# Performance work log

Hardware: AMD Instinct MI355X
Metric: run time of the kernel (lower is better)

The kernel has to match this reference:

```python
import jax, jax.numpy as jnp
import numpy as np

N = 80000
E = 1280000
IN_DIM = 512
OUT_DIM = 64
POS_DIM = 8
NEG_SLOPE = 0.01  # F.leaky_relu default


def setup_inputs() -> dict:
    key = jax.random.key(0)
    k1, k2, k3, k4, k5, k6 = jax.random.split(key, 6)
    h = jax.random.normal(k1, (N, IN_DIM), dtype=jnp.float32)
    pos = jax.random.normal(k2, (N, POS_DIM), dtype=jnp.float32)
    src = jax.random.randint(k3, (E,), 0, N, dtype=jnp.int32)
    dst = jax.random.randint(k4, (E,), 0, N, dtype=jnp.int32)
    W_fc = jax.random.normal(k5, (OUT_DIM, IN_DIM), dtype=jnp.float32) * (1.0 / np.sqrt(IN_DIM))
    W_attn = jax.random.normal(k6, (1, 2 * OUT_DIM + 2 * POS_DIM), dtype=jnp.float32) * 0.1
    return {"h": h, "pos": pos, "src": src, "dst": dst, "W_fc": W_fc, "W_attn": W_attn}


def reference(h, pos, src, dst, W_fc, W_attn):
    # node projection: z = fc(h)  [N, out]
    z = h @ W_fc.T
    # attn_fc applied to concat([z_src, z_dst, pos_src, pos_dst]) == split dot products
    wa = W_attn[0]
    w_zs = wa[:OUT_DIM]
    w_zd = wa[OUT_DIM:2 * OUT_DIM]
    w_ps = wa[2 * OUT_DIM:2 * OUT_DIM + POS_DIM]
    w_pd = wa[2 * OUT_DIM + POS_DIM:]
    el = z @ w_zs + pos @ w_ps  # [N] src-side score
    er = z @ w_zd + pos @ w_pd  # [N] dst-side score
    e = el[src] + er[dst]       # [E]
    e = jnp.where(e > 0, e, NEG_SLOPE * e)  # leaky_relu
    # segment softmax over incoming edges of each dst node (numerically stable)
    emax = jax.ops.segment_max(e, dst, num_segments=N)  # [N]
    ex = jnp.exp(e - emax[dst])                         # [E]
    denom = jax.ops.segment_sum(ex, dst, num_segments=N)  # [N]
    alpha = ex / denom[dst]                             # [E]
    # weighted scatter-sum of src features
    msgs = alpha[:, None] * z[src]                      # [E, out]
    h_out = jax.ops.segment_sum(msgs, dst, num_segments=N)  # [N, out]
    return h_out
```

## Files before the change

kernel.cpp:

```cpp
#include <hip/hip_runtime.h>
#include <math.h>

#define N_NODES 80000
#define E_EDGES 1280000
#define IN_DIM  512
#define OUT_DIM 64
#define POS_DIM 8
#define NEG_SLOPE 0.01f

#define NB_BUCKET 2500
#define BCAP 1024
#define SCAT_CHUNK 4096
#define SCAT_NB 313
#define GEMM_NB 625

#define BM 128
#define BK 64
#define LDA 72
#define LDB 72

typedef __attribute__((ext_vector_type(8))) short short8v;
typedef __attribute__((ext_vector_type(4))) float f32x4;

__device__ __forceinline__ unsigned short f2bf(float f) {
    unsigned u = __float_as_uint(f);
    unsigned r = u + 0x7fff + ((u >> 16) & 1);
    return (unsigned short)(r >> 16);
}
__device__ __forceinline__ float lrelu(float e) { return e > 0.f ? e : NEG_SLOPE * e; }

__global__ __launch_bounds__(256) void gemm_scatter(const float* __restrict__ h,
                                                    const float* __restrict__ W,
                                                    const float* __restrict__ pos,
                                                    const float* __restrict__ Wa,
                                                    const int* __restrict__ src,
                                                    const int* __restrict__ dst,
                                                    char* __restrict__ zq,
                                                    float2* __restrict__ el2,
                                                    float* __restrict__ er,
                                                    int* __restrict__ bcnt,
                                                    int* __restrict__ ebuf) {
    __shared__ __align__(16) char smem[27648];
    const int t = threadIdx.x;

    if (blockIdx.x >= GEMM_NB) {
        int* hh = (int*)smem;
        int* gb = hh + NB_BUCKET;
        const int e0 = (blockIdx.x - GEMM_NB) * SCAT_CHUNK;
        for (int i = t; i < NB_BUCKET; i += 256) hh[i] = 0;
        __syncthreads();

        int key[16];
        short bk[16];
        short lr[16];
        #pragma unroll
        for (int r4 = 0; r4 < 4; ++r4) {
            const int e = e0 + r4 * 1024 + (t << 2);
            if (e + 3 < E_EDGES) {
                const int4 s4 = *(const int4*)&src[e];
                const int4 d4 = *(const int4*)&dst[e];
                bk[r4 * 4 + 0] = (short)(d4.x >> 5); key[r4 * 4 + 0] = (s4.x << 5) | (d4.x & 31);
                lr[r4 * 4 + 0] = (short)atomicAdd(&hh[d4.x >> 5], 1);
                bk[r4 * 4 + 1] = (short)(d4.y >> 5); key[r4 * 4 + 1] = (s4.y << 5) | (d4.y & 31);
                lr[r4 * 4 + 1] = (short)atomicAdd(&hh[d4.y >> 5], 1);
                bk[r4 * 4 + 2] = (short)(d4.z >> 5); key[r4 * 4 + 2] = (s4.z << 5) | (d4.z & 31);
                lr[r4 * 4 + 2] = (short)atomicAdd(&hh[d4.z >> 5], 1);
                bk[r4 * 4 + 3] = (short)(d4.w >> 5); key[r4 * 4 + 3] = (s4.w << 5) | (d4.w & 31);
                lr[r4 * 4 + 3] = (short)atomicAdd(&hh[d4.w >> 5], 1);
            } else {
                #pragma unroll
                for (int j = 0; j < 4; ++j) {
                    const int ee = e + j;
                    if (ee < E_EDGES) {
                        const int d = dst[ee];
                        bk[r4 * 4 + j] = (short)(d >> 5);
                        key[r4 * 4 + j] = (src[ee] << 5) | (d & 31);
                        lr[r4 * 4 + j] = (short)atomicAdd(&hh[d >> 5], 1);
                    } else {
                        bk[r4 * 4 + j] = -1;
                    }
                }
            }
        }
        __syncthreads();

        for (int i = t; i < NB_BUCKET; i += 256) {
            const int c = hh[i];
            gb[i] = c ? (i * BCAP + atomicAdd(&bcnt[i], c)) : 0;
        }
        __syncthreads();

        #pragma unroll
        for (int r = 0; r < 16; ++r) {
            if (bk[r] >= 0) {
                ebuf[gb[bk[r]] + lr[r]] = key[r];
            }
        }
        return;
    }

    unsigned short (*sA)[LDA] = (unsigned short(*)[LDA])smem;
    unsigned short (*sB)[LDB] = (unsigned short(*)[LDB])(smem + BM * LDA * 2);
    const int lane = t & 63;
    const int w    = t >> 6;
    const int row0 = blockIdx.x * BM;
    const int g    = lane >> 4;
    const int rr   = lane & 15;

    f32x4 acc[2][4] = {};
    float4 ra[8];
    float4 rb[4];

    {
        #pragma unroll
        for (int i = 0; i < 8; ++i) {
            const int idx = t + i * 256;
            ra[i] = *(const float4*)&h[(size_t)(row0 + (idx >> 4)) * IN_DIM + ((idx & 15) << 2)];
        }
        #pragma unroll
        for (int i = 0; i < 4; ++i) {
            const int idx = t + i * 256;
            rb[i] = *(const float4*)&W[(size_t)(idx >> 4) * IN_DIM + ((idx & 15) << 2)];
        }
    }

    for (int c = 0; c < IN_DIM / BK; ++c) {
        __syncthreads();
        #pragma unroll
        for (int i = 0; i < 8; ++i) {
            const int idx = t + i * 256;
            ushort4 v = {f2bf(ra[i].x), f2bf(ra[i].y), f2bf(ra[i].z), f2bf(ra[i].w)};
            *(ushort4*)&sA[idx >> 4][(idx & 15) << 2] = v;
        }
        #pragma unroll
        for (int i = 0; i < 4; ++i) {
            const int idx = t + i * 256;
            ushort4 v = {f2bf(rb[i].x), f2bf(rb[i].y), f2bf(rb[i].z), f2bf(rb[i].w)};
            *(ushort4*)&sB[idx >> 4][(idx & 15) << 2] = v;
        }
        __syncthreads();

        if (c < IN_DIM / BK - 1) {
            const int k0 = (c + 1) * BK;
            #pragma unroll
            for (int i = 0; i < 8; ++i) {
                const int idx = t + i * 256;
                ra[i] = *(const float4*)&h[(size_t)(row0 + (idx >> 4)) * IN_DIM + k0 + ((idx & 15) << 2)];
            }
            #pragma unroll
            for (int i = 0; i < 4; ++i) {
                const int idx = t + i * 256;
                rb[i] = *(const float4*)&W[(size_t)(idx >> 4) * IN_DIM + k0 + ((idx & 15) << 2)];
            }
        }

        short8v afr[2][2];
        #pragma unroll
        for (int rt = 0; rt < 2; ++rt)
            #pragma unroll
            for (int ks = 0; ks < 2; ++ks)
                afr[rt][ks] = *(const short8v*)&sA[w * 32 + rt * 16 + rr][ks * 32 + g * 8];
        short8v bfr[4][2];
        #pragma unroll
        for (int ct = 0; ct < 4; ++ct)
            #pragma unroll
            for (int ks = 0; ks < 2; ++ks)
                bfr[ct][ks] = *(const short8v*)&sB[ct * 16 + rr][ks * 32 + g * 8];

        #pragma unroll
        for (int ks = 0; ks < 2; ++ks)
            #pragma unroll
            for (int rt = 0; rt < 2; ++rt)
                #pragma unroll
                for (int ct = 0; ct < 4; ++ct)
                    acc[rt][ct] = __builtin_amdgcn_mfma_f32_16x16x32_bf16(
                        afr[rt][ks], bfr[ct][ks], acc[rt][ct], 0, 0, 0);
    }

    __syncthreads();
    char* sI8 = (char*)sB;

    float wzs_c[4], wzd_c[4];
    #pragma unroll
    for (int ct = 0; ct < 4; ++ct) {
        wzs_c[ct] = Wa[ct * 16 + rr];
        wzd_c[ct] = Wa[OUT_DIM + ct * 16 + rr];
    }
    #pragma unroll
    for (int rt = 0; rt < 2; ++rt)
        #pragma unroll
        for (int r = 0; r < 4; ++r) {
            float pe = 0.f, pd = 0.f, rmax = 0.f;
            #pragma unroll
            for (int ct = 0; ct < 4; ++ct) {
                const float v = acc[rt][ct][r];
                pe += v * wzs_c[ct];
                pd += v * wzd_c[ct];
                rmax = fmaxf(rmax, fabsf(v));
            }
            #pragma unroll
            for (int off = 8; off; off >>= 1) {
                pe += __shfl_xor(pe, off);
                pd += __shfl_xor(pd, off);
                rmax = fmaxf(rmax, __shfl_xor(rmax, off));
            }
            rmax = fmaxf(rmax, 1e-20f);
            const float inv_s = 127.f / rmax;
            const int rloc = w * 32 + rt * 16 + g * 4 + r;
            #pragma unroll
            for (int ct = 0; ct < 4; ++ct) {
                int q = __float2int_rn(acc[rt][ct][r] * inv_s);
                q = max(-127, min(127, q));
                sI8[rloc * 64 + ct * 16 + rr] = (char)q;
            }
            if (rr == 0) {
                const int row = row0 + rloc;
                const float4 p0 = *(const float4*)&pos[(size_t)row * POS_DIM];
                const float4 p1 = *(const float4*)&pos[(size_t)row * POS_DIM + 4];
                const float4 s0 = *(const float4*)&Wa[2 * OUT_DIM];
                const float4 s1 = *(const float4*)&Wa[2 * OUT_DIM + 4];
                const float4 d0 = *(const float4*)&Wa[2 * OUT_DIM + POS_DIM];
                const float4 d1 = *(const float4*)&Wa[2 * OUT_DIM + POS_DIM + 4];
                const float elv = pe + p0.x * s0.x + p0.y * s0.y + p0.z * s0.z + p0.w * s0.w
                                     + p1.x * s1.x + p1.y * s1.y + p1.z * s1.z + p1.w * s1.w;
                el2[row] = make_float2(elv, rmax * (1.f / 127.f));
                er[row] = pd + p0.x * d0.x + p0.y * d0.y + p0.z * d0.z + p0.w * d0.w
                              + p1.x * d1.x + p1.y * d1.y + p1.z * d1.z + p1.w * d1.w;
            }
        }

    __syncthreads();
    uint4* g4 = (uint4*)(zq + (size_t)row0 * 64);
    const uint4* s4 = (const uint4*)sI8;
    g4[t] = s4[t];
    g4[t + 256] = s4[t + 256];
}

__global__ __launch_bounds__(256) void csr_aggregate(const int* __restrict__ ebuf,
                                                     const int* __restrict__ bcnt,
                                                     const float2* __restrict__ el2,
                                                     const float* __restrict__ er,
                                                     const char* __restrict__ zq,
                                                     float* __restrict__ out) {
    __shared__ int sk[BCAP];
    __shared__ int ss[BCAP];
    __shared__ float swt[BCAP];
    __shared__ float ser[32];
    __shared__ float sds[32];
    __shared__ int cnt[32];
    __shared__ int off0[32];
    __shared__ int cur[32];
    const int b = blockIdx.x;
    const int t = threadIdx.x;
    const int lo = b * BCAP;
    const int ne = min(bcnt[b], BCAP);

    if (t < 32) {
        ser[t] = er[(b << 5) + t];
        sds[t] = 0.f;
        cnt[t] = 0;
    }
    __syncthreads();

    const int i4 = t << 2;
    if (i4 < ne) {
        const int4 k4 = *(const int4*)&ebuf[lo + i4];
        sk[i4 + 0] = k4.x; atomicAdd(&cnt[k4.x & 31], 1);
        if (i4 + 1 < ne) { sk[i4 + 1] = k4.y; atomicAdd(&cnt[k4.y & 31], 1); }
        if (i4 + 2 < ne) { sk[i4 + 2] = k4.z; atomicAdd(&cnt[k4.z & 31], 1); }
        if (i4 + 3 < ne) { sk[i4 + 3] = k4.w; atomicAdd(&cnt[k4.w & 31], 1); }
    }
    __syncthreads();

    if (t < 32) {
        const int v = cnt[t];
        int s = v;
        #pragma unroll
        for (int off = 1; off < 32; off <<= 1) {
            const int u = __shfl_up(s, off);
            if (t >= off) s += u;
        }
        off0[t] = s - v;
        cur[t]  = s - v;
    }
    __syncthreads();

    if (i4 < ne) {
        #pragma unroll
        for (int j = 0; j < 4; ++j) {
            if (i4 + j < ne) {
                const int k = sk[i4 + j];
                const int p = atomicAdd(&cur[k & 31], 1);
                ss[p] = k;
            }
        }
    }
    __syncthreads();

    for (int i = t; i < ne; i += 256) {
        const int k = ss[i];
        const int s = k >> 5;
        const int dl = k & 31;
        const float2 v = el2[s];
        const float ex = __expf(lrelu(v.x + ser[dl]));
        atomicAdd(&sds[dl], ex);
        swt[i] = ex * v.y;
        ss[i] = s;
    }
    __syncthreads();

    const int lane = t & 63;
    const int w = t >> 6;
    const int g = lane >> 4;
    const int u = lane & 15;
    for (int r = 0; r < 2; ++r) {
        const int dl = (r << 4) + (w << 2) + g;
        const int d = (b << 5) + dl;
        const int off = off0[dl];
        const int nn = cnt[dl];

        float a0 = 0.f, a1 = 0.f, a2 = 0.f, a3 = 0.f;
        int j = 0;
        for (; j + 8 <= nn; j += 8) {
            float wj[8];
            int sj[8];
            #pragma unroll
            for (int k = 0; k < 8; ++k) {
                wj[k] = swt[off + j + k];
                sj[k] = ss[off + j + k];
            }
            #pragma unroll
            for (int k = 0; k < 8; ++k) {
                const char4 z = *(const char4*)&zq[((size_t)sj[k] << 6) + (u << 2)];
                a0 += wj[k] * (float)z.x; a1 += wj[k] * (float)z.y;
                a2 += wj[k] * (float)z.z; a3 += wj[k] * (float)z.w;
            }
        }
        for (; j < nn; ++j) {
            const float wv = swt[off + j];
            const int sv = ss[off + j];
            const char4 z = *(const char4*)&zq[((size_t)sv << 6) + (u << 2)];
            a0 += wv * (float)z.x; a1 += wv * (float)z.y;
            a2 += wv * (float)z.z; a3 += wv * (float)z.w;
        }

        const float inv = (nn > 0) ? (1.f / sds[dl]) : 0.f;
        f32x4 o = {a0 * inv, a1 * inv, a2 * inv, a3 * inv};
        __builtin_nontemporal_store(o, (f32x4*)&out[((size_t)d << 6) + (u << 2)]);
    }
}

extern "C" void kernel_launch(void* const* d_in, const int* in_sizes, int n_in,
                              void* d_out, int out_size, void* d_ws, size_t ws_size,
                              hipStream_t stream) {
    const float* h   = (const float*)d_in[0];
    const float* pos = (const float*)d_in[1];
    const int* src   = (const int*)d_in[2];
    const int* dst   = (const int*)d_in[3];
    const float* Wfc = (const float*)d_in[4];
    const float* Wa  = (const float*)d_in[5];
    float* out = (float*)d_out;

    char* ws = (char*)d_ws;
    char*   zq   = (char*)  (ws);
    float2* el2  = (float2*)(ws + 5120000);
    float*  er   = (float*) (ws + 5760000);
    int*    ebuf = (int*)   (ws + 6080000);
    int*    bcnt = (int*)   (ws + 16320000);

    hipMemsetAsync(bcnt, 0, NB_BUCKET * sizeof(int), stream);
    gemm_scatter<<<GEMM_NB + SCAT_NB, 256, 0, stream>>>(h, Wfc, pos, Wa, src, dst,
                                                        zq, el2, er, bcnt, ebuf);
    csr_aggregate<<<NB_BUCKET, 256, 0, stream>>>(ebuf, bcnt, el2, er, zq, out);
}
```

Baseline: 81.99 us.

## Fuse edge-weight computation into bucket load and widen per-lane aggregation

The csr_aggregate kernel now computes the exp-weight and softmax denominator while it loads the bucketed edges, and packs weight and source index into a float2. The counting sort then moves these packed pairs, which removes a separate pass and one barrier. The aggregation now gives each destination 8 lanes holding 8 features each instead of 16 lanes holding 4, and handles all 32 destinations in one round instead of two. In exchange it issues two char4 loads per lane per edge rather than one, and gathers with fewer lanes per row.

Result: faster. 79.32 us (-3.3%).

```diff
diff --git a/kernel.cpp b/kernel.cpp
--- a/kernel.cpp
+++ b/kernel.cpp
@@ -242,9 +242,9 @@
                                                      const float* __restrict__ er,
                                                      const char* __restrict__ zq,
                                                      float* __restrict__ out) {
-    __shared__ int sk[BCAP];
-    __shared__ int ss[BCAP];
-    __shared__ float swt[BCAP];
+    __shared__ float2 pk0[BCAP];
+    __shared__ float2 pk1[BCAP];
+    __shared__ unsigned char sdl[BCAP];
     __shared__ float ser[32];
     __shared__ float sds[32];
     __shared__ int cnt[32];
@@ -265,10 +265,21 @@
     const int i4 = t << 2;
     if (i4 < ne) {
         const int4 k4 = *(const int4*)&ebuf[lo + i4];
-        sk[i4 + 0] = k4.x; atomicAdd(&cnt[k4.x & 31], 1);
-        if (i4 + 1 < ne) { sk[i4 + 1] = k4.y; atomicAdd(&cnt[k4.y & 31], 1); }
-        if (i4 + 2 < ne) { sk[i4 + 2] = k4.z; atomicAdd(&cnt[k4.z & 31], 1); }
-        if (i4 + 3 < ne) { sk[i4 + 3] = k4.w; atomicAdd(&cnt[k4.w & 31], 1); }
+        const int kk[4] = {k4.x, k4.y, k4.z, k4.w};
+        #pragma unroll
+        for (int j = 0; j < 4; ++j) {
+            if (i4 + j < ne) {
+                const int k = kk[j];
+                const int s = k >> 5;
+                const int dl = k & 31;
+                const float2 v = el2[s];
+                const float ex = __expf(lrelu(v.x + ser[dl]));
+                atomicAdd(&sds[dl], ex);
+                atomicAdd(&cnt[dl], 1);
+                pk0[i4 + j] = make_float2(ex * v.y, __uint_as_float((unsigned)s));
+                sdl[i4 + j] = (unsigned char)dl;
+            }
+        }
     }
     __syncthreads();
 
@@ -289,65 +300,59 @@
         #pragma unroll
         for (int j = 0; j < 4; ++j) {
             if (i4 + j < ne) {
-                const int k = sk[i4 + j];
-                const int p = atomicAdd(&cur[k & 31], 1);
-                ss[p] = k;
-            }
-        }
-    }
-    __syncthreads();
-
-    for (int i = t; i < ne; i += 256) {
-        const int k = ss[i];
-        const int s = k >> 5;
-        const int dl = k & 31;
-        const float2 v = el2[s];
-        const float ex = __expf(lrelu(v.x + ser[dl]));
-        atomicAdd(&sds[dl], ex);
-        swt[i] = ex * v.y;
-        ss[i] = s;
+                const int dl = sdl[i4 + j];
+                const int p = atomicAdd(&cur[dl], 1);
+                pk1[p] = pk0[i4 + j];
+            }
+        }
     }
     __syncthreads();
 
     const int lane = t & 63;
     const int w = t >> 6;
-    const int g = lane >> 4;
-    const int u = lane & 15;
-    for (int r = 0; r < 2; ++r) {
-        const int dl = (r << 4) + (w << 2) + g;
-        const int d = (b << 5) + dl;
-        const int off = off0[dl];
-        const int nn = cnt[dl];
-
-        float a0 = 0.f, a1 = 0.f, a2 = 0.f, a3 = 0.f;
-        int j = 0;
-        for (; j + 8 <= nn; j += 8) {
-            float wj[8];
-            int sj[8];
-            #pragma unroll
-            for (int k = 0; k < 8; ++k) {
-                wj[k] = swt[off + j + k];
-                sj[k] = ss[off + j + k];
-            }
-            #pragma unroll
-            for (int k = 0; k < 8; ++k) {
-                const char4 z = *(const char4*)&zq[((size_t)sj[k] << 6) + (u << 2)];
-                a0 += wj[k] * (float)z.x; a1 += wj[k] * (float)z.y;
-                a2 += wj[k] * (float)z.z; a3 += wj[k] * (float)z.w;
-            }
-        }
-        for (; j < nn; ++j) {
-            const float wv = swt[off + j];
-            const int sv = ss[off + j];
-            const char4 z = *(const char4*)&zq[((size_t)sv << 6) + (u << 2)];
-            a0 += wv * (float)z.x; a1 += wv * (float)z.y;
-            a2 += wv * (float)z.z; a3 += wv * (float)z.w;
-        }
-
-        const float inv = (nn > 0) ? (1.f / sds[dl]) : 0.f;
-        f32x4 o = {a0 * inv, a1 * inv, a2 * inv, a3 * inv};
-        __builtin_nontemporal_store(o, (f32x4*)&out[((size_t)d << 6) + (u << 2)]);
-    }
+    const int grp = lane >> 3;
+    const int u = lane & 7;
+    const int dl = (w << 3) + grp;
+    const int d = (b << 5) + dl;
+    const int off = off0[dl];
+    const int nn = cnt[dl];
+
+    float a0 = 0.f, a1 = 0.f, a2 = 0.f, a3 = 0.f;
+    float a4 = 0.f, a5 = 0.f, a6 = 0.f, a7 = 0.f;
+    int j = 0;
+    for (; j + 4 <= nn; j += 4) {
+        float2 p[4];
+        #pragma unroll
+        for (int k = 0; k < 4; ++k) p[k] = pk1[off + j + k];
+        #pragma unroll
+        for (int k = 0; k < 4; ++k) {
+            const unsigned sv = __float_as_uint(p[k].y);
+            const float wv = p[k].x;
+            const char4 zA = *(const char4*)&zq[((size_t)sv << 6) + (u << 3)];
+            const char4 zB = *(const char4*)&zq[((size_t)sv << 6) + (u << 3) + 4];
+            a0 += wv * (float)zA.x; a1 += wv * (float)zA.y;
+            a2 += wv * (float)zA.z; a3 += wv * (float)zA.w;
+            a4 += wv * (float)zB.x; a5 += wv * (float)zB.y;
+            a6 += wv * (float)zB.z; a7 += wv * (float)zB.w;
+        }
+    }
+    for (; j < nn; ++j) {
+        const float2 p = pk1[off + j];
+        const unsigned sv = __float_as_uint(p.y);
+        const float wv = p.x;
+        const char4 zA = *(const char4*)&zq[((size_t)sv << 6) + (u << 3)];
+        const char4 zB = *(const char4*)&zq[((size_t)sv << 6) + (u << 3) + 4];
+        a0 += wv * (float)zA.x; a1 += wv * (float)zA.y;
+        a2 += wv * (float)zA.z; a3 += wv * (float)zA.w;
+        a4 += wv * (float)zB.x; a5 += wv * (float)zB.y;
+        a6 += wv * (float)zB.z; a7 += wv * (float)zB.w;
+    }
+
+    const float inv = (nn > 0) ? (1.f / sds[dl]) : 0.f;
+    f32x4 oA = {a0 * inv, a1 * inv, a2 * inv, a3 * inv};
+    f32x4 oB = {a4 * inv, a5 * inv, a6 * inv, a7 * inv};
+    __builtin_nontemporal_store(oA, (f32x4*)&out[((size_t)d << 6) + (u << 3)]);
+    __builtin_nontemporal_store(oB, (f32x4*)&out[((size_t)d << 6) + (u << 3) + 4]);
 }
 
 extern "C" void kernel_launch(void* const* d_in, const int* in_sizes, int n_in,
```
